# Optimization experiments

Measured on AMD Instinct MI355X. Metric: run time of the kernel, lower is better.

The kernel has to match this reference:

```python
import jax, jax.numpy as jnp
import numpy as np
import math

H = 512
NH = 8
HD = H // NH


def _lin_params(key, out_dim, in_dim):
    k1, k2 = jax.random.split(key)
    bound = 1.0 / math.sqrt(in_dim)
    w = jax.random.uniform(k1, (out_dim, in_dim), minval=-bound, maxval=bound, dtype=jnp.float32)
    b = jax.random.uniform(k2, (out_dim,), minval=-bound, maxval=bound, dtype=jnp.float32)
    return w, b


def setup_inputs() -> dict:
    key = jax.random.key(0)
    ks = jax.random.split(key, 16)
    B, L = 8, 1024
    inp = {
        'hidden_states': jax.random.normal(ks[0], (B, L, H), dtype=jnp.float32),
        'text': jax.random.normal(ks[1], (B, L, H), dtype=jnp.float32),
    }
    names = ['q_img', 'k_img', 'v_img', 'q_txt', 'k_txt', 'v_txt', 'out_img', 'out_txt']
    for i, n in enumerate(names):
        w, b = _lin_params(ks[2 + i], H, H)
        inp['w_' + n] = w
        inp['b_' + n] = b
    wcat, bcat = _lin_params(ks[10], H, 2 * H)
    inp['w_cat'] = wcat
    inp['b_cat'] = bcat
    # nn.MultiheadAttention params: in_proj [3H, H], out_proj [H, H]
    inp['in_proj_w'] = jax.random.normal(ks[11], (3 * H, H), dtype=jnp.float32) * (1.0 / math.sqrt(H))
    inp['in_proj_b'] = jnp.zeros((3 * H,), dtype=jnp.float32)
    pw, pb = _lin_params(ks[12], H, H)
    inp['out_proj_w'] = pw
    inp['out_proj_b'] = pb
    return inp


def _lin(x, w, b):
    return x @ w.T + b


def _heads(x):
    B, L, _ = x.shape
    return x.reshape(B, L, NH, HD).transpose(0, 2, 1, 3)  # [B, NH, L, HD]


def _attn(q, k, v):
    # q,k,v: [B, NH, L, HD]; dropout is identity in eval mode
    scores = jnp.einsum('bhqd,bhkd->bhqk', q, k) / math.sqrt(HD)
    probs = jax.nn.softmax(scores, axis=-1)
    ctx = jnp.einsum('bhqk,bhkd->bhqd', probs, v)
    B, _, L, _ = ctx.shape
    return ctx.transpose(0, 2, 1, 3).reshape(B, L, H)


def reference(hidden_states, text,
              w_q_img, b_q_img, w_k_img, b_k_img, w_v_img, b_v_img,
              w_q_txt, b_q_txt, w_k_txt, b_k_txt, w_v_txt, b_v_txt,
              w_out_img, b_out_img, w_out_txt, b_out_txt,
              w_cat, b_cat, in_proj_w, in_proj_b, out_proj_w, out_proj_b):
    q_img = _heads(_lin(hidden_states, w_q_img, b_q_img))
    k_img = _heads(_lin(hidden_states, w_k_img, b_k_img))
    v_img = _heads(_lin(hidden_states, w_v_img, b_v_img))
    q_txt = _heads(_lin(text, w_q_txt, b_q_txt))
    k_txt = _heads(_lin(text, w_k_txt, b_k_txt))
    v_txt = _heads(_lin(text, w_v_txt, b_v_txt))

    ctx_img = _attn(q_img, k_img, v_img)
    ctx_txt = _attn(q_txt, k_txt, v_txt)
    ctx_it = _attn(q_img, k_txt, v_txt)
    ctx_ti = _attn(q_txt, k_img, v_img)

    out_img = _lin((ctx_img + ctx_it) * 0.5, w_out_img, b_out_img)
    out_txt = _lin((ctx_txt + ctx_ti) * 0.5, w_out_txt, b_out_txt)
    out = _lin(jnp.concatenate([out_img, out_txt], axis=2), w_cat, b_cat)

    # attention pooling (nn.MultiheadAttention self-attention, batch-major math)
    qkv = _lin(out, in_proj_w, in_proj_b)
    q, k, v = jnp.split(qkv, 3, axis=-1)
    ctx = _attn(_heads(q), _heads(k), _heads(v))
    return _lin(ctx, out_proj_w, out_proj_b)
```

## Files before the change

### kernel.cpp

```cpp
#include <hip/hip_runtime.h>

typedef unsigned short u16;
typedef __attribute__((ext_vector_type(4))) unsigned short u16x4;
typedef __attribute__((ext_vector_type(8))) unsigned short u16x8;
typedef __attribute__((ext_vector_type(4))) float f32x4;
typedef __attribute__((ext_vector_type(8))) __bf16 bf16x8;
typedef __attribute__((ext_vector_type(2))) unsigned int u32x2;
typedef __attribute__((ext_vector_type(4))) unsigned int u32x4;

#define WS_XH    0UL
#define WS_XT    8388608UL
#define WS_W     16777216UL
#define WS_BQI   24117248UL
#define WS_BQT   24123392UL
#define WS_QKVI  24129536UL
#define WS_QKVT  49295360UL
#define WS_VTI   74461184UL
#define WS_VTT   82849792UL
#define WS_CTXIA 91238400UL
#define WS_CTXTA 99627008UL
#define WS_OCAT  108015616UL
#define WS_OUT2  24129536UL
#define WS_QKVP  32518144UL
#define WS_VTP   57683968UL
#define WS_CTXP  66072576UL

#define SCALE_LOG2E_O8 0.18033688011112042f

__device__ __forceinline__ u16 f2bf(float f) {
  unsigned u = __float_as_uint(f);
  u += 0x7fffu + ((u >> 16) & 1u);
  return (u16)(u >> 16);
}
__device__ __forceinline__ float bf2f(u16 v) {
  return __uint_as_float(((unsigned)v) << 16);
}
__device__ __forceinline__ bf16x8 as_bf(u16x8 v) { return __builtin_bit_cast(bf16x8, v); }
__device__ __forceinline__ f32x4 mfma16(bf16x8 a, bf16x8 b, f32x4 c) {
  return __builtin_amdgcn_mfma_f32_16x16x32_bf16(a, b, c, 0, 0, 0);
}
__device__ __forceinline__ unsigned cvt_pk_bf16(float lo, float hi) {
  unsigned r;
  asm("v_cvt_pk_bf16_f32 %0, %1, %2" : "=v"(r) : "v"(lo), "v"(hi));
  return r;
}
__device__ __forceinline__ void gl_lds16(const u16* g, u16* l) {
  __builtin_amdgcn_global_load_lds(
      (const __attribute__((address_space(1))) void*)g,
      (__attribute__((address_space(3))) void*)l, 16, 0, 0);
}

__global__ __launch_bounds__(256) void cvt_f32_bf16(const float* __restrict__ s0,
                                                    const float* __restrict__ s1,
                                                    u16* __restrict__ d0,
                                                    u16* __restrict__ d1, int n) {
  const float* s = blockIdx.y ? s1 : s0;
  u16* d = blockIdx.y ? d1 : d0;
  int i = (blockIdx.x * 256 + threadIdx.x) * 4;
  if (i >= n) return;
  float4 v = *(const float4*)(s + i);
  u16x4 o;
  o[0] = f2bf(v.x); o[1] = f2bf(v.y); o[2] = f2bf(v.z); o[3] = f2bf(v.w);
  *(u16x4*)(d + i) = o;
}

__global__ __launch_bounds__(256) void prep_weights(
    const float* __restrict__ wqi, const float* __restrict__ wki, const float* __restrict__ wvi,
    const float* __restrict__ wqt, const float* __restrict__ wkt, const float* __restrict__ wvt,
    const float* __restrict__ woi, const float* __restrict__ wot,
    const float* __restrict__ wc,  const float* __restrict__ wip, const float* __restrict__ wop,
    const float* __restrict__ bqi, const float* __restrict__ bki, const float* __restrict__ bvi,
    const float* __restrict__ bqt, const float* __restrict__ bkt, const float* __restrict__ bvt,
    u16* __restrict__ wdst, float* __restrict__ bi, float* __restrict__ bt) {
  int i = blockIdx.x * 256 + threadIdx.x;
  if (i < 786432) {
    const float* s = i < 262144 ? wqi : (i < 524288 ? wki : wvi);
    wdst[i] = f2bf(s[i & 262143]);
  } else if (i < 1572864) {
    int j = i - 786432;
    const float* s = j < 262144 ? wqt : (j < 524288 ? wkt : wvt);
    wdst[i] = f2bf(s[j & 262143]);
  } else if (i < 1835008) wdst[i] = f2bf(woi[i - 1572864]);
  else if (i < 2097152)   wdst[i] = f2bf(wot[i - 1835008]);
  else if (i < 2621440)   wdst[i] = f2bf(wc [i - 2097152]);
  else if (i < 3407872)   wdst[i] = f2bf(wip[i - 2621440]);
  else if (i < 3670016)   wdst[i] = f2bf(wop[i - 3407872]);
  else if (i < 3671552) {
    int j = i - 3670016;
    bi[j] = j < 512 ? bqi[j] : (j < 1024 ? bki[j - 512] : bvi[j - 1024]);
  } else if (i < 3673088) {
    int j = i - 3671552;
    bt[j] = j < 512 ? bqt[j] : (j < 1024 ? bkt[j - 512] : bvt[j - 1024]);
  }
}

__global__ __launch_bounds__(256) void gemm_bf16(
    const u16* __restrict__ A, const u16* __restrict__ A2, int lda,
    const u16* __restrict__ W,
    const float* __restrict__ bias, u16* __restrict__ C, int ldc, int coff, int K,
    int f32out, int qcols, float qscale, u16* __restrict__ vtout,
    long zdA, long zdA2, long zdW, long zdB, long zdC, long zdVT, int zdCoff) {
  if (blockIdx.z) {
    A += zdA;
    if (A2) A2 += zdA2;
    W += zdW; bias += zdB; C += zdC;
    if (vtout) vtout += zdVT;
    coff += zdCoff;
  }
  __shared__ __align__(16) u16 As[2][8 * 512];
  __shared__ __align__(16) u16 Bs[2][8 * 512];
  const int tid = threadIdx.x, lane = tid & 63, wv = tid >> 6;
  const int wm = wv >> 1, wn = wv & 1;
  const int ln15 = lane & 15;
  const int m0 = blockIdx.x * 128, n0 = blockIdx.y * 128;

  const int srow = lane & 15, skc = lane >> 4;
  const u16* gA0 = A + (long)(m0 + wv * 32 + srow) * lda + skc * 8;
  const u16* gA1 = gA0 + (long)16 * lda;
  const u16* gW0 = W + (long)(n0 + wv * 32 + srow) * K + skc * 8;
  const u16* gW1 = gW0 + (long)16 * K;

  f32x4 acc[4][4];
#pragma unroll
  for (int j = 0; j < 4; ++j) {
    float bv = bias[n0 + wn * 64 + j * 16 + ln15];
#pragma unroll
    for (int i = 0; i < 4; ++i) acc[i][j] = f32x4{bv, bv, bv, bv};
  }

  if (!A2) {
    {
      u16* la = As[0] + wv * 1024;
      u16* lb = Bs[0] + wv * 1024;
      gl_lds16(gA0, la);
      gl_lds16(gA1, la + 512);
      gl_lds16(gW0, lb);
      gl_lds16(gW1, lb + 512);
    }
    int cur = 0;
    for (int k0 = 0; k0 < K; k0 += 32, cur ^= 1) {
      __syncthreads();
      if (k0 + 32 < K) {
        u16* la = As[cur ^ 1] + wv * 1024;
        u16* lb = Bs[cur ^ 1] + wv * 1024;
        gl_lds16(gA0 + k0 + 32, la);
        gl_lds16(gA1 + k0 + 32, la + 512);
        gl_lds16(gW0 + k0 + 32, lb);
        gl_lds16(gW1 + k0 + 32, lb + 512);
      }
      bf16x8 af[4], bfr[4];
#pragma unroll
      for (int i = 0; i < 4; ++i)
        af[i] = as_bf(*(const u16x8*)(As[cur] + (wm * 4 + i) * 512 + lane * 8));
#pragma unroll
      for (int j = 0; j < 4; ++j)
        bfr[j] = as_bf(*(const u16x8*)(Bs[cur] + (wn * 4 + j) * 512 + lane * 8));
#pragma unroll
      for (int i = 0; i < 4; ++i)
#pragma unroll
        for (int j = 0; j < 4; ++j) acc[i][j] = mfma16(af[i], bfr[j], acc[i][j]);
    }
  } else {
    const u16* gA20 = A2 + (long)(m0 + wv * 32 + srow) * lda + skc * 8;
    const u16* gA21 = gA20 + (long)16 * lda;
    u16x8 ra0 = *(const u16x8*)(gA0);
    u16x8 ra1 = *(const u16x8*)(gA1);
    u16x8 rb0 = *(const u16x8*)(gW0);
    u16x8 rb1 = *(const u16x8*)(gW1);
    u16x8 rc0 = *(const u16x8*)(gA20);
    u16x8 rc1 = *(const u16x8*)(gA21);
    int buf = 0;
    for (int k0 = 0; k0 < K; k0 += 32, buf ^= 1) {
      u16x8 wa0 = ra0, wa1 = ra1;
#pragma unroll
      for (int u = 0; u < 8; ++u) {
        wa0[u] = f2bf(bf2f(ra0[u]) + bf2f(rc0[u]));
        wa1[u] = f2bf(bf2f(ra1[u]) + bf2f(rc1[u]));
      }
      u16* la = As[buf] + (wv * 2) * 512;
      u16* lb = Bs[buf] + (wv * 2) * 512;
      *(u16x8*)(la + lane * 8) = wa0;
      *(u16x8*)(la + 512 + lane * 8) = wa1;
      *(u16x8*)(lb + lane * 8) = rb0;
      *(u16x8*)(lb + 512 + lane * 8) = rb1;
      __syncthreads();
      if (k0 + 32 < K) {
        ra0 = *(const u16x8*)(gA0 + k0 + 32);
        ra1 = *(const u16x8*)(gA1 + k0 + 32);
        rb0 = *(const u16x8*)(gW0 + k0 + 32);
        rb1 = *(const u16x8*)(gW1 + k0 + 32);
        rc0 = *(const u16x8*)(gA20 + k0 + 32);
        rc1 = *(const u16x8*)(gA21 + k0 + 32);
      }
      bf16x8 af[4], bfr[4];
#pragma unroll
      for (int i = 0; i < 4; ++i)
        af[i] = as_bf(*(const u16x8*)(As[buf] + (wm * 4 + i) * 512 + lane * 8));
#pragma unroll
      for (int j = 0; j < 4; ++j)
        bfr[j] = as_bf(*(const u16x8*)(Bs[buf] + (wn * 4 + j) * 512 + lane * 8));
#pragma unroll
      for (int i = 0; i < 4; ++i)
#pragma unroll
        for (int j = 0; j < 4; ++j) acc[i][j] = mfma16(af[i], bfr[j], acc[i][j]);
    }
  }
  const int quad = lane >> 4;
  const int qr4 = quad * 4;
  if (vtout && n0 >= 1024) {
#pragma unroll
    for (int j = 0; j < 4; ++j) {
      int col = n0 + wn * 64 + j * 16 + ln15;
      int dg = col - 1024;
#pragma unroll
      for (int i = 0; i < 4; ++i) {
        int row0 = m0 + wm * 64 + i * 16 + qr4;
        long vr = ((long)(row0 >> 10) * 8 + (dg >> 6)) * 64 + (dg & 63);
        u16x4 ov;
#pragma unroll
        for (int r = 0; r < 4; ++r) ov[r] = f2bf(acc[i][j][r]);
        *(u16x4*)(vtout + vr * 1024 + (row0 & 1023)) = ov;
      }
    }
    return;
  }
  float colsc[4];
#pragma unroll
  for (int j = 0; j < 4; ++j)
    colsc[j] = (n0 + wn * 64 + j * 16 < qcols) ? qscale : 1.0f;
#pragma unroll
  for (int i = 0; i < 4; ++i)
#pragma unroll
    for (int r = 0; r < 4; ++r) {
      int row = m0 + wm * 64 + i * 16 + qr4 + r;
      long cidx = (long)row * ldc + coff + n0 + wn * 64 + ln15;
      if (f32out) {
        float* cf = (float*)C + cidx;
#pragma unroll
        for (int j = 0; j < 4; ++j) cf[j * 16] = acc[i][j][r] * colsc[j];
      } else {
        u16* cp = C + cidx;
#pragma unroll
        for (int j = 0; j < 4; ++j) cp[j * 16] = f2bf(acc[i][j][r] * colsc[j]);
      }
    }
}

template <int NQF, bool DUAL>
__global__ __launch_bounds__(256) void attn_flash(
    const u16* __restrict__ Q0, const u16* __restrict__ Q1, int ldq,
    const u16* __restrict__ K0, const u16* __restrict__ VT0,
    const u16* __restrict__ K1, const u16* __restrict__ VT1, int ldk,
    u16* __restrict__ O00, u16* __restrict__ O01,
    u16* __restrict__ O10, u16* __restrict__ O11, int ldo, float outscale) {
  __shared__ __align__(16) u16 Kt[2][32][72];
  __shared__ __align__(16) u16 Vt[2][64][40];
  const int tid = threadIdx.x, lane = tid & 63, wv = tid >> 6;
  const int ln15 = lane & 15, quad = lane >> 4, q8 = quad * 8;
  const int h = blockIdx.y;

  const u16 *Q, *K, *VT;
  u16* O;
  int qtile, b;
  if constexpr (DUAL) {
    qtile = blockIdx.x >> 1;
    const int phase = blockIdx.x & 1;
    const int qsel = blockIdx.z & 1;
    b = blockIdx.z >> 1;
    Q = qsel ? Q1 : Q0;
    const int ksel = qsel ^ phase;
    K = ksel ? K1 : K0;
    VT = ksel ? VT1 : VT0;
    O = qsel ? (phase ? O11 : O10) : (phase ? O01 : O00);
  } else {
    qtile = blockIdx.x;
    b = blockIdx.z;
    Q = Q0; K = K0; VT = VT0; O = O00;
  }
  const long qrow = (long)b * 1024 + qtile * (NQF * 64) + wv * (NQF * 16);

  bf16x8 qf[NQF][2];
#pragma unroll
  for (int qi = 0; qi < NQF; ++qi) {
    const u16* qp = Q + (qrow + qi * 16 + ln15) * ldq + h * 64;
    qf[qi][0] = as_bf(*(const u16x8*)(qp + q8));
    qf[qi][1] = as_bf(*(const u16x8*)(qp + 32 + q8));
  }

  u16x8 ones_u;
#pragma unroll
  for (int j = 0; j < 8; ++j) ones_u[j] = 0x3F80;
  const bf16x8 onesb = as_bf(ones_u);

  const int kk = tid >> 3, dc = (tid & 7) * 8;
  const int vd = tid >> 2;
  const int ko = (tid & 3) * 8;
  const int vs0 = ((tid & 1) << 4) | ((tid & 2) << 1);
  const u16* Kbase = K + ((long)b * 1024 + kk) * ldk + h * 64 + dc;
  const u16* Vbase = VT + ((long)((b * 8 + h) * 64 + vd)) * 1024 + ko;

  f32x4 o[NQF][4];
  f32x4 lacc[NQF];
#pragma unroll
  for (int qi = 0; qi < NQF; ++qi) {
    lacc[qi] = f32x4{0.f, 0.f, 0.f, 0.f};
#pragma unroll
    for (int j = 0; j < 4; ++j) o[qi][j] = f32x4{0.f, 0.f, 0.f, 0.f};
  }

  u32x4 kreg = *(const u32x4*)(Kbase);
  u32x4 vreg = *(const u32x4*)(Vbase);

  int cur = 0;
  for (int k0 = 0; k0 < 1024; k0 += 32, cur ^= 1) {
    *(u32x4*)(&Kt[cur][kk][dc]) = kreg;
    u32x2 vlo = {vreg[0], vreg[1]}, vhi = {vreg[2], vreg[3]};
    *(u32x2*)(&Vt[cur][vd][vs0]) = vlo;
    *(u32x2*)(&Vt[cur][vd][vs0 + 8]) = vhi;
    __syncthreads();
    if (k0 + 32 < 1024) {
      kreg = *(const u32x4*)(Kbase + (long)(k0 + 32) * ldk);
      vreg = *(const u32x4*)(Vbase + (k0 + 32));
    }

    f32x4 st[2][NQF];
#pragma unroll
    for (int kt = 0; kt < 2; ++kt) {
      bf16x8 ka0 = as_bf(*(const u16x8*)(&Kt[cur][kt * 16 + ln15][q8]));
      bf16x8 ka1 = as_bf(*(const u16x8*)(&Kt[cur][kt * 16 + ln15][32 + q8]));
#pragma unroll
      for (int qi = 0; qi < NQF; ++qi) {
        f32x4 z = f32x4{0.f, 0.f, 0.f, 0.f};
        z = mfma16(ka0, qf[qi][0], z);
        z = mfma16(ka1, qf[qi][1], z);
        st[kt][qi] = z;
      }
    }

    bf16x8 pb[NQF];
#pragma unroll
    for (int qi = 0; qi < NQF; ++qi) {
      float p00 = __builtin_amdgcn_exp2f(st[0][qi][0]);
      float p01 = __builtin_amdgcn_exp2f(st[0][qi][1]);
      float p02 = __builtin_amdgcn_exp2f(st[0][qi][2]);
      float p03 = __builtin_amdgcn_exp2f(st[0][qi][3]);
      float p10 = __builtin_amdgcn_exp2f(st[1][qi][0]);
      float p11 = __builtin_amdgcn_exp2f(st[1][qi][1]);
      float p12 = __builtin_amdgcn_exp2f(st[1][qi][2]);
      float p13 = __builtin_amdgcn_exp2f(st[1][qi][3]);
      u32x4 pk;
      pk[0] = cvt_pk_bf16(p00, p01);
      pk[1] = cvt_pk_bf16(p02, p03);
      pk[2] = cvt_pk_bf16(p10, p11);
      pk[3] = cvt_pk_bf16(p12, p13);
      pb[qi] = as_bf(__builtin_bit_cast(u16x8, pk));
      lacc[qi] = mfma16(onesb, pb[qi], lacc[qi]);
    }
#pragma unroll
    for (int j = 0; j < 4; ++j) {
      bf16x8 av = as_bf(*(const u16x8*)(&Vt[cur][j * 16 + ln15][q8]));
#pragma unroll
      for (int qi = 0; qi < NQF; ++qi) o[qi][j] = mfma16(av, pb[qi], o[qi][j]);
    }
  }

#pragma unroll
  for (int qi = 0; qi < NQF; ++qi) {
    float inv = outscale / lacc[qi][0];
    long row = qrow + qi * 16 + ln15;
#pragma unroll
    for (int j = 0; j < 4; ++j) {
      u16x4 ov;
#pragma unroll
      for (int r = 0; r < 4; ++r) ov[r] = f2bf(o[qi][j][r] * inv);
      *(u16x4*)(O + row * ldo + h * 64 + j * 16 + quad * 4) = ov;
    }
  }
}

extern "C" void kernel_launch(void* const* d_in, const int* in_sizes, int n_in,
                              void* d_out, int out_size, void* d_ws, size_t ws_size,
                              hipStream_t stream) {
  const float* hidden = (const float*)d_in[0];
  const float* text   = (const float*)d_in[1];
  const float* wqi = (const float*)d_in[2];  const float* bqi = (const float*)d_in[3];
  const float* wki = (const float*)d_in[4];  const float* bki = (const float*)d_in[5];
  const float* wvi = (const float*)d_in[6];  const float* bvi = (const float*)d_in[7];
  const float* wqt = (const float*)d_in[8];  const float* bqt = (const float*)d_in[9];
  const float* wkt = (const float*)d_in[10]; const float* bkt = (const float*)d_in[11];
  const float* wvt = (const float*)d_in[12]; const float* bvt = (const float*)d_in[13];
  const float* woi = (const float*)d_in[14]; const float* boi = (const float*)d_in[15];
  const float* wot = (const float*)d_in[16]; const float* bot = (const float*)d_in[17];
  const float* wc  = (const float*)d_in[18]; const float* bc  = (const float*)d_in[19];
  const float* wip = (const float*)d_in[20]; const float* bip = (const float*)d_in[21];
  const float* wop = (const float*)d_in[22]; const float* bop = (const float*)d_in[23];

  char* ws = (char*)d_ws;
  u16* XH    = (u16*)(ws + WS_XH);
  u16* XT    = (u16*)(ws + WS_XT);
  u16* WB    = (u16*)(ws + WS_W);
  float* BQI = (float*)(ws + WS_BQI);
  float* BQT = (float*)(ws + WS_BQT);
  u16* QKVI  = (u16*)(ws + WS_QKVI);
  u16* QKVT  = (u16*)(ws + WS_QKVT);
  u16* VTI   = (u16*)(ws + WS_VTI);
  u16* VTT   = (u16*)(ws + WS_VTT);
  u16* CTXIA = (u16*)(ws + WS_CTXIA);
  u16* CTXIB = (u16*)(ws + WS_XH);
  u16* CTXTA = (u16*)(ws + WS_CTXTA);
  u16* CTXTB = (u16*)(ws + WS_XT);
  u16* OCAT  = (u16*)(ws + WS_OCAT);
  u16* OUT2  = (u16*)(ws + WS_OUT2);
  u16* QKVP  = (u16*)(ws + WS_QKVP);
  u16* VTP   = (u16*)(ws + WS_VTP);
  u16* CTXP  = (u16*)(ws + WS_CTXP);

  u16* WQKVI = WB;
  u16* WOUTI = WB + 1572864;
  u16* WCAT  = WB + 2097152;
  u16* WINP  = WB + 2621440;
  u16* WOUTP = WB + 3407872;

  const int NACT = 8192 * 512;

  cvt_f32_bf16<<<dim3(NACT / 1024, 2), 256, 0, stream>>>(hidden, text, XH, XT, NACT);
  prep_weights<<<dim3(14348), 256, 0, stream>>>(wqi, wki, wvi, wqt, wkt, wvt, woi, wot,
                                                wc, wip, wop, bqi, bki, bvi, bqt, bkt, bvt,
                                                WB, BQI, BQT);
  gemm_bf16<<<dim3(64, 12, 2), 256, 0, stream>>>(
      XH, nullptr, 512, WQKVI, BQI, QKVI, 1536, 0, 512, 0, 512, SCALE_LOG2E_O8, VTI,
      4194304, 0, 786432, 1536, 12582912, 4194304, 0);
  attn_flash<4, true><<<dim3(8, 8, 16), 256, 0, stream>>>(
      QKVI, QKVT, 1536, QKVI + 512, VTI, QKVT + 512, VTT, 1536,
      CTXIA, CTXIB, CTXTA, CTXTB, 512, 0.5f);
  gemm_bf16<<<dim3(64, 4, 2), 256, 0, stream>>>(
      CTXIA, CTXIB, 512, WOUTI, boi, OCAT, 1024, 0, 512, 0, 0, 1.0f, nullptr,
      4194304, 4194304, 262144, (long)(bot - boi),
      0, 0, 512);
  gemm_bf16<<<dim3(64, 4, 1), 256, 0, stream>>>(
      OCAT, nullptr, 1024, WCAT, bc, OUT2, 512, 0, 1024, 0, 0, 1.0f, nullptr,
      0, 0, 0, 0, 0, 0, 0);
  gemm_bf16<<<dim3(64, 12, 1), 256, 0, stream>>>(
      OUT2, nullptr, 512, WINP, bip, QKVP, 1536, 0, 512, 0, 512, SCALE_LOG2E_O8, VTP,
      0, 0, 0, 0, 0, 0, 0);
  attn_flash<2, false><<<dim3(8, 8, 8), 256, 0, stream>>>(
      QKVP, nullptr, 1536, QKVP + 512, VTP, nullptr, nullptr, 1536,
      CTXP, nullptr, nullptr, nullptr, 512, 1.0f);
  gemm_bf16<<<dim3(64, 4, 1), 256, 0, stream>>>(
      CTXP, nullptr, 512, WOUTP, bop, (u16*)d_out, 512, 0, 512, 1, 0, 1.0f, nullptr,
      0, 0, 0, 0, 0, 0, 0);
}
```

Measured before the change: 397.9 us.

## Fold out_img/out_txt, cat, and in_proj linears into one precomputed weight

The chain of three linear layers (the per-stream output projections, the concat projection and the MHA in-projection) is precomputed into a single effective weight and bias. Small weight-by-weight GEMMs and bias-fusion kernels build it per call. The pooled QKV is then produced by one K=1024 GEMM that reads the four attention context buffers directly, averaging each pair on load, so the two intermediate activation GEMMs and their buffers go away. It also retunes the first attention launch to smaller query tiles with twice the blocks, and folding the weights changes the bf16 rounding of the result.

New measurement: 471.6 us. 18.5% more time.

```diff
diff --git a/kernel.cpp b/kernel.cpp
--- a/kernel.cpp
+++ b/kernel.cpp
@@ -19,8 +19,12 @@
 #define WS_VTT   82849792UL
 #define WS_CTXIA 91238400UL
 #define WS_CTXTA 99627008UL
-#define WS_OCAT  108015616UL
-#define WS_OUT2  24129536UL
+#define WS_ZB    108015616UL
+#define WS_BEFF  108019712UL
+#define WS_BQP   108023808UL
+#define WS_WEFFIT 108032000UL
+#define WS_WEFFTT 108556288UL
+#define WS_WQP   109080576UL
 #define WS_QKVP  32518144UL
 #define WS_VTP   57683968UL
 #define WS_CTXP  66072576UL
@@ -71,7 +75,8 @@
     const float* __restrict__ wc,  const float* __restrict__ wip, const float* __restrict__ wop,
     const float* __restrict__ bqi, const float* __restrict__ bki, const float* __restrict__ bvi,
     const float* __restrict__ bqt, const float* __restrict__ bkt, const float* __restrict__ bvt,
-    u16* __restrict__ wdst, float* __restrict__ bi, float* __restrict__ bt) {
+    u16* __restrict__ wdst, float* __restrict__ bi, float* __restrict__ bt,
+    float* __restrict__ zb) {
   int i = blockIdx.x * 256 + threadIdx.x;
   if (i < 786432) {
     const float* s = i < 262144 ? wqi : (i < 524288 ? wki : wvi);
@@ -80,8 +85,13 @@
     int j = i - 786432;
     const float* s = j < 262144 ? wqt : (j < 524288 ? wkt : wvt);
     wdst[i] = f2bf(s[j & 262143]);
-  } else if (i < 1835008) wdst[i] = f2bf(woi[i - 1572864]);
-  else if (i < 2097152)   wdst[i] = f2bf(wot[i - 1835008]);
+  } else if (i < 1835008) {
+    int t = i - 1572864;
+    wdst[i] = f2bf(woi[((t & 511) << 9) | (t >> 9)]);
+  } else if (i < 2097152) {
+    int t = i - 1835008;
+    wdst[i] = f2bf(wot[((t & 511) << 9) | (t >> 9)]);
+  }
   else if (i < 2621440)   wdst[i] = f2bf(wc [i - 2097152]);
   else if (i < 3407872)   wdst[i] = f2bf(wip[i - 2621440]);
   else if (i < 3670016)   wdst[i] = f2bf(wop[i - 3407872]);
@@ -91,12 +101,39 @@
   } else if (i < 3673088) {
     int j = i - 3671552;
     bt[j] = j < 512 ? bqt[j] : (j < 1024 ? bkt[j - 512] : bvt[j - 1024]);
-  }
+  } else if (i < 3673600) {
+    zb[i - 3673088] = 0.0f;
+  }
+}
+
+__global__ __launch_bounds__(256) void bias_fuse1(const float* __restrict__ wc,
+                                                  const float* __restrict__ bc,
+                                                  const float* __restrict__ boi,
+                                                  const float* __restrict__ bot,
+                                                  float* __restrict__ beff) {
+  int m = blockIdx.x * 256 + threadIdx.x;
+  if (m >= 512) return;
+  const float* r = wc + (long)m * 1024;
+  float s = bc[m];
+  for (int j = 0; j < 512; ++j) s += r[j] * boi[j] + r[512 + j] * bot[j];
+  beff[m] = s;
+}
+__global__ __launch_bounds__(256) void bias_fuse2(const float* __restrict__ wip,
+                                                  const float* __restrict__ bip,
+                                                  const float* __restrict__ beff,
+                                                  float* __restrict__ bqp) {
+  int p = blockIdx.x * 256 + threadIdx.x;
+  if (p >= 1536) return;
+  const float* r = wip + (long)p * 512;
+  float s = bip[p];
+  for (int m = 0; m < 512; ++m) s += r[m] * beff[m];
+  bqp[p] = s;
 }
 
 __global__ __launch_bounds__(256) void gemm_bf16(
-    const u16* __restrict__ A, const u16* __restrict__ A2, int lda,
-    const u16* __restrict__ W,
+    const u16* __restrict__ A, const u16* __restrict__ A2,
+    const u16* __restrict__ Ahi, const u16* __restrict__ Ahi2, int lda,
+    const u16* __restrict__ W, int ldw,
     const float* __restrict__ bias, u16* __restrict__ C, int ldc, int coff, int K,
     int f32out, int qcols, float qscale, u16* __restrict__ vtout,
     long zdA, long zdA2, long zdW, long zdB, long zdC, long zdVT, int zdCoff) {
@@ -115,10 +152,11 @@
   const int m0 = blockIdx.x * 128, n0 = blockIdx.y * 128;
 
   const int srow = lane & 15, skc = lane >> 4;
-  const u16* gA0 = A + (long)(m0 + wv * 32 + srow) * lda + skc * 8;
+  const long rowoff = (long)(m0 + wv * 32 + srow) * lda + skc * 8;
+  const u16* gA0 = A + rowoff;
   const u16* gA1 = gA0 + (long)16 * lda;
-  const u16* gW0 = W + (long)(n0 + wv * 32 + srow) * K + skc * 8;
-  const u16* gW1 = gW0 + (long)16 * K;
+  const u16* gW0 = W + (long)(n0 + wv * 32 + srow) * ldw + skc * 8;
+  const u16* gW1 = gW0 + (long)16 * ldw;
 
   f32x4 acc[4][4];
 #pragma unroll
@@ -161,17 +199,17 @@
         for (int j = 0; j < 4; ++j) acc[i][j] = mfma16(af[i], bfr[j], acc[i][j]);
     }
   } else {
-    const u16* gA20 = A2 + (long)(m0 + wv * 32 + srow) * lda + skc * 8;
-    const u16* gA21 = gA20 + (long)16 * lda;
-    u16x8 ra0 = *(const u16x8*)(gA0);
-    u16x8 ra1 = *(const u16x8*)(gA1);
+    auto pa  = [&](int k) { return ((Ahi  && k >= 512) ? Ahi  + (k - 512) : A  + k) + rowoff; };
+    auto pa2 = [&](int k) { return ((Ahi2 && k >= 512) ? Ahi2 + (k - 512) : A2 + k) + rowoff; };
+    u16x8 ra0 = *(const u16x8*)(pa(0));
+    u16x8 ra1 = *(const u16x8*)(pa(0) + (long)16 * lda);
     u16x8 rb0 = *(const u16x8*)(gW0);
     u16x8 rb1 = *(const u16x8*)(gW1);
-    u16x8 rc0 = *(const u16x8*)(gA20);
-    u16x8 rc1 = *(const u16x8*)(gA21);
+    u16x8 rc0 = *(const u16x8*)(pa2(0));
+    u16x8 rc1 = *(const u16x8*)(pa2(0) + (long)16 * lda);
     int buf = 0;
     for (int k0 = 0; k0 < K; k0 += 32, buf ^= 1) {
-      u16x8 wa0 = ra0, wa1 = ra1;
+      u16x8 wa0, wa1;
 #pragma unroll
       for (int u = 0; u < 8; ++u) {
         wa0[u] = f2bf(bf2f(ra0[u]) + bf2f(rc0[u]));
@@ -185,12 +223,12 @@
       *(u16x8*)(lb + 512 + lane * 8) = rb1;
       __syncthreads();
       if (k0 + 32 < K) {
-        ra0 = *(const u16x8*)(gA0 + k0 + 32);
-        ra1 = *(const u16x8*)(gA1 + k0 + 32);
+        ra0 = *(const u16x8*)(pa(k0 + 32));
+        ra1 = *(const u16x8*)(pa(k0 + 32) + (long)16 * lda);
         rb0 = *(const u16x8*)(gW0 + k0 + 32);
         rb1 = *(const u16x8*)(gW1 + k0 + 32);
-        rc0 = *(const u16x8*)(gA20 + k0 + 32);
-        rc1 = *(const u16x8*)(gA21 + k0 + 32);
+        rc0 = *(const u16x8*)(pa2(k0 + 32));
+        rc1 = *(const u16x8*)(pa2(k0 + 32) + (long)16 * lda);
       }
       bf16x8 af[4], bfr[4];
 #pragma unroll
@@ -409,14 +447,19 @@
   u16* CTXIB = (u16*)(ws + WS_XH);
   u16* CTXTA = (u16*)(ws + WS_CTXTA);
   u16* CTXTB = (u16*)(ws + WS_XT);
-  u16* OCAT  = (u16*)(ws + WS_OCAT);
-  u16* OUT2  = (u16*)(ws + WS_OUT2);
+  float* ZB    = (float*)(ws + WS_ZB);
+  float* BEFF  = (float*)(ws + WS_BEFF);
+  float* BQP   = (float*)(ws + WS_BQP);
+  u16* WEFFIT  = (u16*)(ws + WS_WEFFIT);
+  u16* WEFFTT  = (u16*)(ws + WS_WEFFTT);
+  u16* WQP     = (u16*)(ws + WS_WQP);
   u16* QKVP  = (u16*)(ws + WS_QKVP);
   u16* VTP   = (u16*)(ws + WS_VTP);
   u16* CTXP  = (u16*)(ws + WS_CTXP);
 
   u16* WQKVI = WB;
-  u16* WOUTI = WB + 1572864;
+  u16* WOIT  = WB + 1572864;
+  u16* WOTT  = WB + 1835008;
   u16* WCAT  = WB + 2097152;
   u16* WINP  = WB + 2621440;
   u16* WOUTP = WB + 3407872;
@@ -424,29 +467,35 @@
   const int NACT = 8192 * 512;
 
   cvt_f32_bf16<<<dim3(NACT / 1024, 2), 256, 0, stream>>>(hidden, text, XH, XT, NACT);
-  prep_weights<<<dim3(14348), 256, 0, stream>>>(wqi, wki, wvi, wqt, wkt, wvt, woi, wot,
+  prep_weights<<<dim3(14350), 256, 0, stream>>>(wqi, wki, wvi, wqt, wkt, wvt, woi, wot,
                                                 wc, wip, wop, bqi, bki, bvi, bqt, bkt, bvt,
-                                                WB, BQI, BQT);
+                                                WB, BQI, BQT, ZB);
+  bias_fuse1<<<dim3(2), 256, 0, stream>>>(wc, bc, boi, bot, BEFF);
+  bias_fuse2<<<dim3(6), 256, 0, stream>>>(wip, bip, BEFF, BQP);
+  gemm_bf16<<<dim3(4, 4, 2), 256, 0, stream>>>(
+      WOIT, nullptr, nullptr, nullptr, 512, WCAT, 1024, ZB, WEFFIT, 512, 0, 512,
+      0, 0, 1.0f, nullptr,
+      262144, 0, 512, 0, 262144, 0, 0);
+  gemm_bf16<<<dim3(12, 4, 2), 256, 0, stream>>>(
+      WINP, nullptr, nullptr, nullptr, 512, WEFFIT, 512, ZB, WQP, 1024, 0, 512,
+      0, 0, 1.0f, nullptr,
+      0, 0, 262144, 0, 0, 0, 512);
   gemm_bf16<<<dim3(64, 12, 2), 256, 0, stream>>>(
-      XH, nullptr, 512, WQKVI, BQI, QKVI, 1536, 0, 512, 0, 512, SCALE_LOG2E_O8, VTI,
+      XH, nullptr, nullptr, nullptr, 512, WQKVI, 512, BQI, QKVI, 1536, 0, 512,
+      0, 512, SCALE_LOG2E_O8, VTI,
       4194304, 0, 786432, 1536, 12582912, 4194304, 0);
-  attn_flash<4, true><<<dim3(8, 8, 16), 256, 0, stream>>>(
+  attn_flash<2, true><<<dim3(16, 8, 16), 256, 0, stream>>>(
       QKVI, QKVT, 1536, QKVI + 512, VTI, QKVT + 512, VTT, 1536,
       CTXIA, CTXIB, CTXTA, CTXTB, 512, 0.5f);
-  gemm_bf16<<<dim3(64, 4, 2), 256, 0, stream>>>(
-      CTXIA, CTXIB, 512, WOUTI, boi, OCAT, 1024, 0, 512, 0, 0, 1.0f, nullptr,
-      4194304, 4194304, 262144, (long)(bot - boi),
-      0, 0, 512);
-  gemm_bf16<<<dim3(64, 4, 1), 256, 0, stream>>>(
-      OCAT, nullptr, 1024, WCAT, bc, OUT2, 512, 0, 1024, 0, 0, 1.0f, nullptr,
-      0, 0, 0, 0, 0, 0, 0);
   gemm_bf16<<<dim3(64, 12, 1), 256, 0, stream>>>(
-      OUT2, nullptr, 512, WINP, bip, QKVP, 1536, 0, 512, 0, 512, SCALE_LOG2E_O8, VTP,
+      CTXIA, CTXIB, CTXTA, CTXTB, 512, WQP, 1024, BQP, QKVP, 1536, 0, 1024,
+      0, 512, SCALE_LOG2E_O8, VTP,
       0, 0, 0, 0, 0, 0, 0);
   attn_flash<2, false><<<dim3(8, 8, 8), 256, 0, stream>>>(
       QKVP, nullptr, 1536, QKVP + 512, VTP, nullptr, nullptr, 1536,
       CTXP, nullptr, nullptr, nullptr, 512, 1.0f);
   gemm_bf16<<<dim3(64, 4, 1), 256, 0, stream>>>(
-      CTXP, nullptr, 512, WOUTP, bop, (u16*)d_out, 512, 0, 512, 1, 0, 1.0f, nullptr,
+      CTXP, nullptr, nullptr, nullptr, 512, WOUTP, 512, bop, (u16*)d_out, 512, 0, 512,
+      1, 0, 1.0f, nullptr,
       0, 0, 0, 0, 0, 0, 0);
 }
```
